# Optimization experiments

Hardware: AMD Instinct MI355X
Metric: run time of the kernel (lower is better)

The kernel has to match this reference:

```python
import jax, jax.numpy as jnp
from jax import lax
import numpy as np

B, IMG, PS = 64, 384, 16
DM, DS, DI = 96, 16, 96
DT_RANK = 6
NREP = 4
NCLS = 5
HP = IMG // PS            # 24 patches per side
N = HP * HP               # 576 tokens


def _ln(x, g, b):
    m = x.mean(-1, keepdims=True)
    v = ((x - m) ** 2).mean(-1, keepdims=True)
    return (x - m) * lax.rsqrt(v + 1e-5) * g + b


def setup_inputs() -> dict:
    key = jax.random.key(0)
    ks = jax.random.split(key, 16)
    nrm = lambda k, s: jax.random.normal(k, s, jnp.float32) * 0.02
    return {
        "x": jax.random.uniform(ks[0], (B, 3, IMG, IMG), jnp.float32),
        "W_pe": nrm(ks[1], (DM, 3, PS, PS)), "b_pe": jnp.zeros((DM,), jnp.float32),
        "W_vis": nrm(ks[2], (DM, 1)), "b_vis": jnp.zeros((1,), jnp.float32),
        "dn_g": jnp.ones((DM,), jnp.float32), "dn_b": jnp.zeros((DM,), jnp.float32),
        "W_gate": nrm(ks[3], (DM, DM)), "b_gate": jnp.zeros((DM,), jnp.float32),
        "ln_g": jnp.ones((DM,), jnp.float32), "ln_b": jnp.zeros((DM,), jnp.float32),
        "W_in": nrm(ks[4], (DM, 2 * DI)),
        "conv_w": nrm(ks[5], (DI, 1, 3)),
        "W_xproj": nrm(ks[6], (DI, DT_RANK + 2 * DS)),
        "W_dt": nrm(ks[7], (DT_RANK, DI)), "b_dt": jnp.full((DI,), -2.0, jnp.float32),
        "A_log": jnp.log(jnp.tile(jnp.arange(1, DS + 1, dtype=jnp.float32), (DI, 1))),
        "D": jnp.ones((DI,), jnp.float32),
        "W_out": nrm(ks[8], (DI, DM)),
        "hd_dw": nrm(ks[9], (DM, 1, 3, 3)),
        "bn_g": jnp.ones((DM,), jnp.float32), "bn_b": jnp.zeros((DM,), jnp.float32),
        "bn_m": jnp.zeros((DM,), jnp.float32), "bn_v": jnp.ones((DM,), jnp.float32),
        "W_heat": nrm(ks[10], (NCLS, DM)), "b_heat": jnp.full((NCLS,), -2.19, jnp.float32),
        "W_off": nrm(ks[11], (2, DM)), "b_off": jnp.zeros((2,), jnp.float32),
        "W_size": nrm(ks[12], (2, DM)), "b_size": jnp.zeros((2,), jnp.float32),
    }


def _forward(x, W_pe, b_pe, W_vis, b_vis, dn_g, dn_b, W_gate, b_gate,
             ln_g, ln_b, W_in, conv_w, W_xproj, W_dt, b_dt, A_log, D, W_out,
             hd_dw, bn_g, bn_b, bn_m, bn_v, W_heat, b_heat, W_off, b_off, W_size, b_size):
    # --- retinex preprocessing (single-scale, log domain) ---
    kblur = jnp.ones((3, 1, 5, 5), jnp.float32) / 25.0
    L = lax.conv_general_dilated(x, kblur, (1, 1), 'SAME',
                                 feature_group_count=3,
                                 dimension_numbers=('NCHW', 'OIHW', 'NCHW'))
    x = jnp.log1p(jnp.clip(x, 0.0)) - jnp.log1p(jnp.clip(L, 0.0))
    # --- patch embedding: strided conv -> tokens (B,N,DM) ---
    t = lax.conv_general_dilated(x, W_pe, (PS, PS), 'VALID',
                                 dimension_numbers=('NCHW', 'OIHW', 'NCHW'))
    t = t + b_pe[None, :, None, None]
    tokens = t.reshape(B, DM, N).transpose(0, 2, 1)
    # --- visibility estimator: per-token gate (B,N,1) ---
    vis = jax.nn.sigmoid(tokens @ W_vis + b_vis)
    # --- dual norm: LN + sigmoid gate ---
    tokens = _ln(tokens, dn_g, dn_b)
    norm_gate = jax.nn.sigmoid(tokens @ W_gate + b_gate)  # (B,N,DM)
    # --- weight-shared NC-SSM blocks ---
    A = -jnp.exp(A_log)  # (DI,DS)
    for _ in range(NREP):
        resid = tokens
        h = _ln(tokens, ln_g, ln_b)
        xz = h @ W_in                      # (B,N,2*DI)
        xin, z = xz[..., :DI], xz[..., DI:]
        # causal depthwise conv1d over sequence, kernel 3
        xc = xin.transpose(0, 2, 1)        # (B,DI,N)
        xc = lax.conv_general_dilated(xc, conv_w, (1,), [(2, 0)],
                                      feature_group_count=DI,
                                      dimension_numbers=('NCH', 'OIH', 'NCH'))
        xs = jax.nn.silu(xc.transpose(0, 2, 1))  # (B,N,DI)
        # selective-scan parameters
        proj = xs @ W_xproj                # (B,N,DT_RANK+2*DS)
        dt_raw = proj[..., :DT_RANK]
        Bc = proj[..., DT_RANK:DT_RANK + DS]
        Cc = proj[..., DT_RANK + DS:]
        dt = jax.nn.softplus(dt_raw @ W_dt + b_dt)  # (B,N,DI)
        # time-major scan
        def step(hst, inp):
            dt_t, B_t, C_t, x_t = inp      # (B,DI),(B,DS),(B,DS),(B,DI)
            dA = jnp.exp(dt_t[:, :, None] * A)                 # (B,DI,DS)
            hst = dA * hst + (dt_t * x_t)[:, :, None] * B_t[:, None, :]
            y = jnp.einsum('bds,bs->bd', hst, C_t)
            return hst, y
        h0 = jnp.zeros((B, DI, DS), jnp.float32)
        _, ys = lax.scan(step, h0, (dt.transpose(1, 0, 2), Bc.transpose(1, 0, 2),
                                    Cc.transpose(1, 0, 2), xs.transpose(1, 0, 2)))
        y = ys.transpose(1, 0, 2) + D * xs           # (B,N,DI)
        y = y * jax.nn.silu(z) * vis                  # gated by z and visibility
        tokens = resid + (y @ W_out) * norm_gate
    # --- CenterNet-style head ---
    f = tokens.transpose(0, 2, 1).reshape(B, DM, HP, HP)
    g = lax.conv_general_dilated(f, hd_dw, (1, 1), 'SAME',
                                 feature_group_count=DM,
                                 dimension_numbers=('NCHW', 'OIHW', 'NCHW'))
    g = (g - bn_m[None, :, None, None]) * lax.rsqrt(bn_v + 1e-5)[None, :, None, None]
    g = jax.nn.silu(g * bn_g[None, :, None, None] + bn_b[None, :, None, None])
    heat = jnp.einsum('bchw,oc->bohw', g, W_heat) + b_heat[None, :, None, None]
    off = jnp.einsum('bchw,oc->bohw', f, W_off) + b_off[None, :, None, None]
    size = jnp.einsum('bchw,oc->bohw', f, W_size) + b_size[None, :, None, None]
    return heat, off, size


def reference(x, W_pe, b_pe, W_vis, b_vis, dn_g, dn_b, W_gate, b_gate,
              ln_g, ln_b, W_in, conv_w, W_xproj, W_dt, b_dt, A_log, D, W_out,
              hd_dw, bn_g, bn_b, bn_m, bn_v, W_heat, b_heat, W_off, b_off, W_size, b_size):
    return _forward(x, W_pe, b_pe, W_vis, b_vis, dn_g, dn_b, W_gate, b_gate,
                    ln_g, ln_b, W_in, conv_w, W_xproj, W_dt, b_dt, A_log, D, W_out,
                    hd_dw, bn_g, bn_b, bn_m, bn_v, W_heat, b_heat, W_off, b_off,
                    W_size, b_size)
```

## Files before the change

### kernel.cpp

```cpp
#include <hip/hip_runtime.h>

#define DEVINL __device__ __forceinline__

typedef __attribute__((ext_vector_type(8))) short bf8v;
typedef __attribute__((ext_vector_type(4))) float f4v;

DEVINL float b2f(unsigned short u){ union{unsigned int i; float f;} x; x.i = ((unsigned int)u)<<16; return x.f; }
DEVINL unsigned short f2b(float f){ union{float f; unsigned int i;} x; x.f = f; unsigned int r = x.i + 0x7FFFu + ((x.i>>16)&1u); return (unsigned short)(r>>16); }
DEVINL float sigf(float v){ return 1.f/(1.f + __expf(-v)); }
DEVINL void unpack8(const uint4 u, float* d){
  d[0]=b2f((unsigned short)(u.x)); d[1]=b2f((unsigned short)(u.x>>16));
  d[2]=b2f((unsigned short)(u.y)); d[3]=b2f((unsigned short)(u.y>>16));
  d[4]=b2f((unsigned short)(u.z)); d[5]=b2f((unsigned short)(u.z>>16));
  d[6]=b2f((unsigned short)(u.w)); d[7]=b2f((unsigned short)(u.w>>16));
}
DEVINL uint4 pack8(const float* s){
  uint4 u;
  u.x = (unsigned int)f2b(s[0]) | ((unsigned int)f2b(s[1])<<16);
  u.y = (unsigned int)f2b(s[2]) | ((unsigned int)f2b(s[3])<<16);
  u.z = (unsigned int)f2b(s[4]) | ((unsigned int)f2b(s[5])<<16);
  u.w = (unsigned int)f2b(s[6]) | ((unsigned int)f2b(s[7])<<16);
  return u;
}
union FragU { uint4 u; bf8v v; };


#define WS_XLOG   ((size_t)0)
#define WS_TOKRAW ((size_t)56623104)
#define WS_VIS    ((size_t)70778880)
#define WS_WGT    ((size_t)70926336)
#define WS_WIT    ((size_t)70944768)
#define WS_WXT    ((size_t)70981632)
#define WS_WOT    ((size_t)71006208)
#define WS_AMAT   ((size_t)71024640)
#define WS_WPE    ((size_t)71030784)
#define WS_CW     ((size_t)71178240)
#define WS_TOK    ((size_t)0)
#define WS_GATE   ((size_t)14155776)
#define WS_XSB    ((size_t)21233664)
#define WS_Y2     ((size_t)28311552)
#define WS_XIN    ((size_t)35389440)
#define WS_ZSV    ((size_t)42467328)
#define WS_DT     ((size_t)49545216)
#define WS_BC     ((size_t)56623104)

#define PREP_STRIDE (128*256)
__global__ __launch_bounds__(256) void k_prep(
    const float* __restrict__ Wgate, const float* __restrict__ Win,
    const float* __restrict__ Wxproj, const float* __restrict__ Wdt,
    const float* __restrict__ Wout, const float* __restrict__ Alog,
    const float* __restrict__ Wpe, const float* __restrict__ convw,
    unsigned short* __restrict__ WgT, unsigned short* __restrict__ WiT,
    unsigned short* __restrict__ WxT, unsigned short* __restrict__ WoT,
    float* __restrict__ Amat, unsigned short* __restrict__ WpeB,
    float* __restrict__ cwsplit)
{
  int gtid = blockIdx.x*256 + threadIdx.x;
  for (int i = gtid; i < 9216; i += PREP_STRIDE){
    int n = i/96, k = i - n*96;
    WgT[n*96+k] = f2b(Wgate[k*96+n]);
    WoT[n*96+k] = f2b(Wout[k*96+n]);
  }
  for (int i = gtid; i < 18432; i += PREP_STRIDE){
    int n = i/96, k = i - n*96;
    WiT[n*96+k] = f2b(Win[k*192+n]);
  }
  for (int i = gtid; i < 12288; i += PREP_STRIDE){
    int n = i/96, k = i - n*96;
    if (n < 96){
      float s = 0.f;
      for (int r = 0; r < 6; ++r) s += Wxproj[k*38+r] * Wdt[r*96+n];
      WxT[n*96+k] = f2b(s);
    } else {
      WxT[n*96+k] = f2b(Wxproj[k*38 + 6 + (n-96)]);
    }
  }
  for (int i = gtid; i < 1536; i += PREP_STRIDE) Amat[i] = -__expf(Alog[i]);
  for (int i = gtid; i < 73728; i += PREP_STRIDE) WpeB[i] = f2b(Wpe[i]);
  for (int i = gtid; i < 96; i += PREP_STRIDE){
    cwsplit[i]       = convw[i*3+0];
    cwsplit[96+i]    = convw[i*3+1];
    cwsplit[192+i]   = convw[i*3+2];
  }
}

__global__ __launch_bounds__(256) void k_blur(const float* __restrict__ x,
                                              unsigned short* __restrict__ xlog)
{
  __shared__ float xt[12*384];
  int bid = blockIdx.x;
  int tile = bid % 48; int bc = bid / 48; int c = bc % 3; int b = bc / 3;
  const float* xin = x + (size_t)(b*3 + c) * 147456;
  unsigned short* xout = xlog + (size_t)(b*3 + c) * 147456;
  int y0 = tile * 8;
  int tid = threadIdx.x;

  #pragma unroll
  for (int k = 0; k < 5; ++k){
    int idx = tid + k*256;
    if (idx < 1152){
      int r = idx / 96; int c4 = idx - r*96;
      int gy = y0 - 2 + r;
      float4 v = make_float4(0.f,0.f,0.f,0.f);
      if (gy >= 0 && gy < 384) v = *(const float4*)(xin + gy*384 + c4*4);
      *(float4*)(xt + r*384 + c4*4) = v;
    }
  }
  __syncthreads();

  #pragma unroll
  for (int k = 0; k < 2; ++k){
    int slot = tid + k*256;
    int r = slot >> 6; int c8 = slot & 63;
    bool act = (c8 < 48);
    float vs[8];
    if (act){
      const float* base = xt + r*384 + c8*8;
      float4 a0 = *(const float4*)(base);
      float4 a1 = *(const float4*)(base + 4);
      vs[0]=a0.x; vs[1]=a0.y; vs[2]=a0.z; vs[3]=a0.w;
      vs[4]=a1.x; vs[5]=a1.y; vs[6]=a1.z; vs[7]=a1.w;
      #pragma unroll
      for (int i = 1; i < 5; ++i){
        float4 p = *(const float4*)(base + i*384);
        float4 q = *(const float4*)(base + i*384 + 4);
        vs[0]+=p.x; vs[1]+=p.y; vs[2]+=p.z; vs[3]+=p.w;
        vs[4]+=q.x; vs[5]+=q.y; vs[6]+=q.z; vs[7]+=q.w;
      }
    } else {
      #pragma unroll
      for (int j = 0; j < 8; ++j) vs[j] = 0.f;
    }
    float l2 = __shfl_up(vs[6], 1);
    float l1 = __shfl_up(vs[7], 1);
    float r1 = __shfl_down(vs[0], 1);
    float r2 = __shfl_down(vs[1], 1);
    if (c8 == 0){ l2 = 0.f; l1 = 0.f; }
    if (c8 == 47){ r1 = 0.f; r2 = 0.f; }
    if (act){
      float e[12];
      e[0]=l2; e[1]=l1;
      #pragma unroll
      for (int j = 0; j < 8; ++j) e[2+j] = vs[j];
      e[10]=r1; e[11]=r2;
      const float* xraw = xt + (r+2)*384 + c8*8;
      float xv[8];
      *(float4*)(xv)   = *(const float4*)(xraw);
      *(float4*)(xv+4) = *(const float4*)(xraw + 4);
      float res[8];
      #pragma unroll
      for (int j = 0; j < 8; ++j){
        float s = ((e[j]+e[j+1]) + (e[j+2]+e[j+3])) + e[j+4];
        float L = fmaxf(s * 0.04f, 0.f);
        float xc = fmaxf(xv[j], 0.f);
        res[j] = __logf(1.f + xc) - __logf(1.f + L);
      }
      *(uint4*)(xout + (y0+r)*384 + c8*8) = pack8(res);
    }
  }
}

__global__ __launch_bounds__(256) void k_patch(const unsigned short* __restrict__ xlog,
    const unsigned short* __restrict__ WpeB, const float* __restrict__ bpe,
    float* __restrict__ tokraw)
{
  int wid = threadIdx.x >> 6, lane = threadIdx.x & 63;
  int gid = blockIdx.x*4 + wid;
  int tile = gid >> 1, half = gid & 1;
  int m0 = tile*16;
  int nf0 = half*3;
  int l15 = lane & 15, q = lane >> 4;
  int ma0 = m0 + l15;
  int b0 = ma0/576; int r0 = ma0 - b0*576; int hp0 = r0/24; int wp0 = r0 - hp0*24;
  size_t base0 = (size_t)b0*442368 + (size_t)hp0*6144 + (size_t)wp0*16;
  f4v acc[3];
  #pragma unroll
  for (int j=0;j<3;++j)
    #pragma unroll
    for (int r=0;r<4;++r) acc[j][r] = 0.f;
  for (int ks = 0; ks < 24; ++ks){
    int k0 = ks*32 + q*8;
    int c  = k0 >> 8;
    int ph = (k0 >> 4) & 15;
    int pw = k0 & 15;
    size_t off = (size_t)c*147456 + (size_t)ph*384 + pw;
    bf8v a0 = *(const bf8v*)(xlog + base0 + off);
    #pragma unroll
    for (int nf = 0; nf < 3; ++nf){
      bf8v bb = *(const bf8v*)(WpeB + (size_t)((nf0+nf)*16 + l15)*768 + k0);
      acc[nf] = __builtin_amdgcn_mfma_f32_16x16x32_bf16(a0, bb, acc[nf], 0, 0, 0);
    }
  }
  #pragma unroll
  for (int nf=0; nf<3; ++nf)
    #pragma unroll
    for (int r=0; r<4; ++r){
      int m = m0 + q*4 + r;
      int n = (nf0+nf)*16 + l15;
      tokraw[(size_t)m*96 + n] = acc[nf][r] + bpe[n];
    }
}

__global__ __launch_bounds__(256) void k_lngate(const float* __restrict__ in,
    const float* __restrict__ g, const float* __restrict__ bta,
    const float* __restrict__ Wvis, const float* __restrict__ bvis,
    const unsigned short* __restrict__ BT, const float* __restrict__ bg,
    float* __restrict__ tokout, unsigned short* __restrict__ gate,
    float* __restrict__ vis)
{
  int wid = threadIdx.x >> 6, lane = threadIdx.x & 63;
  int gid = blockIdx.x*4 + wid;
  int tile = gid >> 1, half = gid & 1;
  int m0 = tile*16;
  int nf0 = half*3;
  int l15 = lane & 15, q = lane >> 4;
  int ma0 = m0 + l15;
  float a0v[24];
  float s0=0.f, w0=0.f, vd=0.f;
  #pragma unroll
  for (int ks = 0; ks < 3; ++ks){
    int k0 = ks*32 + q*8;
    #pragma unroll
    for (int h = 0; h < 2; ++h){
      float4 va = *(const float4*)(in + (size_t)ma0*96 + k0 + h*4);
      float4 wv = *(const float4*)(Wvis + k0 + h*4);
      int o = ks*8 + h*4;
      a0v[o+0]=va.x; a0v[o+1]=va.y; a0v[o+2]=va.z; a0v[o+3]=va.w;
      s0 += (va.x+va.y)+(va.z+va.w);
      w0 += (va.x*va.x+va.y*va.y)+(va.z*va.z+va.w*va.w);
      vd += (va.x*wv.x+va.y*wv.y)+(va.z*wv.z+va.w*wv.w);
    }
  }
  s0 += __shfl_xor(s0, 16); s0 += __shfl_xor(s0, 32);
  w0 += __shfl_xor(w0, 16); w0 += __shfl_xor(w0, 32);
  vd += __shfl_xor(vd, 16); vd += __shfl_xor(vd, 32);
  float mu0 = s0*(1.f/96.f);
  float rs0 = rsqrtf(fmaxf(w0*(1.f/96.f)-mu0*mu0, 0.f) + 1e-5f);
  if (half == 0 && q == 0) vis[ma0] = sigf(vd + bvis[0]);

  bf8v fa0[3];
  #pragma unroll
  for (int ks = 0; ks < 3; ++ks){
    int k0 = ks*32 + q*8;
    float gv[8], bv[8];
    *(float4*)(gv)   = *(const float4*)(g + k0);
    *(float4*)(gv+4) = *(const float4*)(g + k0 + 4);
    *(float4*)(bv)   = *(const float4*)(bta + k0);
    *(float4*)(bv+4) = *(const float4*)(bta + k0 + 4);
    float v0[8];
    #pragma unroll
    for (int j = 0; j < 8; ++j){
      v0[j] = (a0v[ks*8+j]-mu0)*rs0*gv[j] + bv[j];
    }
    if (half == 0){
      *(float4*)(tokout + (size_t)ma0*96 + k0)     = make_float4(v0[0],v0[1],v0[2],v0[3]);
      *(float4*)(tokout + (size_t)ma0*96 + k0 + 4) = make_float4(v0[4],v0[5],v0[6],v0[7]);
    }
    FragU U0; U0.u = pack8(v0);
    fa0[ks] = U0.v;
  }

  f4v acc[3];
  #pragma unroll
  for (int j=0;j<3;++j)
    #pragma unroll
    for (int r=0;r<4;++r) acc[j][r] = 0.f;
  const bf8v* bp = (const bf8v*)(BT) + (size_t)l15*12 + q;
  #pragma unroll
  for (int ks = 0; ks < 3; ++ks){
    #pragma unroll
    for (int nf = 0; nf < 3; ++nf){
      bf8v bb = bp[(nf0+nf)*192 + ks*4];
      acc[nf] = __builtin_amdgcn_mfma_f32_16x16x32_bf16(fa0[ks], bb, acc[nf], 0, 0, 0);
    }
  }
  #pragma unroll
  for (int nf=0; nf<3; ++nf)
    #pragma unroll
    for (int r=0; r<4; ++r){
      int m = m0 + q*4 + r;
      int n = (nf0+nf)*16 + l15;
      gate[(size_t)m*96 + n] = f2b(sigf(acc[nf][r] + bg[n]));
    }
}

template<int NF, class Epi>
__global__ __launch_bounds__(256) void tokgemm96(const unsigned short* __restrict__ A,
    const unsigned short* __restrict__ BT, Epi epi)
{
  constexpr int NF2 = NF/2;
  int wid = threadIdx.x >> 6, lane = threadIdx.x & 63;
  int gid = blockIdx.x*4 + wid;
  int tile = gid >> 1, half = gid & 1;
  int m0 = tile*16;
  int nf0 = half*NF2;
  int l15 = lane & 15, q = lane >> 4;
  f4v acc[NF2];
  #pragma unroll
  for (int j=0;j<NF2;++j)
    #pragma unroll
    for (int r=0;r<4;++r) acc[j][r] = 0.f;
  const bf8v* a0p = (const bf8v*)(A) + (size_t)(m0 + l15)*12 + q;
  const bf8v* bp  = (const bf8v*)(BT) + (size_t)l15*12 + q;
  #pragma unroll
  for (int ks = 0; ks < 3; ++ks){
    bf8v a0 = a0p[ks*4];
    #pragma unroll
    for (int nf = 0; nf < NF2; ++nf){
      bf8v bb = bp[(nf0+nf)*192 + ks*4];
      acc[nf] = __builtin_amdgcn_mfma_f32_16x16x32_bf16(a0, bb, acc[nf], 0, 0, 0);
    }
  }
  #pragma unroll
  for (int nf=0; nf<NF2; ++nf)
    #pragma unroll
    for (int r=0; r<4; ++r)
      epi(m0 + q*4 + r, (nf0+nf)*16 + l15, acc[nf][r]);
}

struct WoutEpi {
  const unsigned short* gate; float* tokens;
  __device__ void operator()(int m, int n, float v) const {
    size_t i = (size_t)m*96 + n;
    tokens[i] = tokens[i] + v * b2f(gate[i]);
  }
};

__global__ __launch_bounds__(256) void k_lnwin(const float* __restrict__ tokp,
    const float* __restrict__ lng, const float* __restrict__ lnb,
    const unsigned short* __restrict__ BT, const float* __restrict__ vis,
    unsigned short* __restrict__ xin, unsigned short* __restrict__ zsv)
{
  int wid = threadIdx.x >> 6, lane = threadIdx.x & 63;
  int gid = blockIdx.x*4 + wid;
  int tile = gid >> 1, half = gid & 1;
  int m0 = tile*16;
  int nf0 = half*6;
  int l15 = lane & 15, q = lane >> 4;
  int ma0 = m0 + l15;
  float a0v[24];
  float s0=0.f, w0=0.f;
  #pragma unroll
  for (int ks = 0; ks < 3; ++ks){
    int k0 = ks*32 + q*8;
    #pragma unroll
    for (int h = 0; h < 2; ++h){
      float4 va = *(const float4*)(tokp + (size_t)ma0*96 + k0 + h*4);
      int o = ks*8 + h*4;
      a0v[o+0]=va.x; a0v[o+1]=va.y; a0v[o+2]=va.z; a0v[o+3]=va.w;
      s0 += (va.x+va.y)+(va.z+va.w);
      w0 += (va.x*va.x+va.y*va.y)+(va.z*va.z+va.w*va.w);
    }
  }
  s0 += __shfl_xor(s0, 16); s0 += __shfl_xor(s0, 32);
  w0 += __shfl_xor(w0, 16); w0 += __shfl_xor(w0, 32);
  float mu0 = s0*(1.f/96.f);
  float rs0 = rsqrtf(fmaxf(w0*(1.f/96.f)-mu0*mu0, 0.f) + 1e-5f);

  bf8v fa0[3];
  #pragma unroll
  for (int ks = 0; ks < 3; ++ks){
    int k0 = ks*32 + q*8;
    float gv[8], bv[8];
    *(float4*)(gv)   = *(const float4*)(lng + k0);
    *(float4*)(gv+4) = *(const float4*)(lng + k0 + 4);
    *(float4*)(bv)   = *(const float4*)(lnb + k0);
    *(float4*)(bv+4) = *(const float4*)(lnb + k0 + 4);
    float v0[8];
    #pragma unroll
    for (int j = 0; j < 8; ++j){
      v0[j] = (a0v[ks*8+j]-mu0)*rs0*gv[j] + bv[j];
    }
    FragU U0; U0.u = pack8(v0);
    fa0[ks] = U0.v;
  }

  f4v acc[6];
  #pragma unroll
  for (int j=0;j<6;++j)
    #pragma unroll
    for (int r=0;r<4;++r) acc[j][r] = 0.f;
  const bf8v* bp = (const bf8v*)(BT) + (size_t)l15*12 + q;
  #pragma unroll
  for (int ks = 0; ks < 3; ++ks){
    #pragma unroll
    for (int nf = 0; nf < 6; ++nf){
      bf8v bb = bp[(nf0+nf)*192 + ks*4];
      acc[nf] = __builtin_amdgcn_mfma_f32_16x16x32_bf16(fa0[ks], bb, acc[nf], 0, 0, 0);
    }
  }
  if (half == 0){
    #pragma unroll
    for (int nf=0; nf<6; ++nf)
      #pragma unroll
      for (int r=0; r<4; ++r){
        int m = m0 + q*4 + r;
        int n = nf*16 + l15;
        xin[(size_t)m*96 + n] = f2b(acc[nf][r]);
      }
  } else {
    #pragma unroll
    for (int nf=0; nf<6; ++nf)
      #pragma unroll
      for (int r=0; r<4; ++r){
        int m = m0 + q*4 + r;
        int n = (6+nf)*16 + l15;
        float v = acc[nf][r];
        float s = v * sigf(v);
        zsv[(size_t)m*96 + (n-96)] = f2b(s * vis[m]);
      }
  }
}

__global__ __launch_bounds__(256) void k_convxp(const unsigned short* __restrict__ xinb,
    const float* __restrict__ cwsplit, const unsigned short* __restrict__ BT,
    const float* __restrict__ bdt, unsigned short* __restrict__ xsb,
    unsigned short* __restrict__ dt, unsigned short* __restrict__ bc)
{
  int wid = threadIdx.x >> 6, lane = threadIdx.x & 63;
  int gid = blockIdx.x*4 + wid;
  int tile = gid >> 1, half = gid & 1;
  int m0 = tile*16;
  int nf0 = half*4;
  int l15 = lane & 15, q = lane >> 4;
  int ma0 = m0 + l15;
  int t0 = ma0 % 576;
  const float* cw0 = cwsplit;
  const float* cw1 = cwsplit + 96;
  const float* cw2 = cwsplit + 192;

  bf8v fa0[3];
  uint4 z4 = make_uint4(0,0,0,0);
  #pragma unroll
  for (int ks = 0; ks < 3; ++ks){
    int k0 = ks*32 + q*8;
    const unsigned short* r0p = xinb + (size_t)ma0*96 + k0;
    uint4 c0u  = *(const uint4*)(r0p);
    uint4 p10u = (t0 >= 1) ? *(const uint4*)(r0p - 96)  : z4;
    uint4 p20u = (t0 >= 2) ? *(const uint4*)(r0p - 192) : z4;
    float fc0[8], fp10[8], fp20[8];
    unpack8(c0u, fc0); unpack8(p10u, fp10); unpack8(p20u, fp20);
    float w0v[8], w1v[8], w2v[8];
    *(float4*)(w0v)   = *(const float4*)(cw0 + k0);
    *(float4*)(w0v+4) = *(const float4*)(cw0 + k0 + 4);
    *(float4*)(w1v)   = *(const float4*)(cw1 + k0);
    *(float4*)(w1v+4) = *(const float4*)(cw1 + k0 + 4);
    *(float4*)(w2v)   = *(const float4*)(cw2 + k0);
    *(float4*)(w2v+4) = *(const float4*)(cw2 + k0 + 4);
    float xs0[8];
    #pragma unroll
    for (int j = 0; j < 8; ++j){
      float v0 = w2v[j]*fc0[j] + w1v[j]*fp10[j] + w0v[j]*fp20[j];
      xs0[j] = v0 * sigf(v0);
    }
    FragU U0; U0.u = pack8(xs0);
    fa0[ks] = U0.v;
    if (half == 0) *(uint4*)(xsb + (size_t)ma0*96 + k0) = U0.u;
  }

  f4v acc[4];
  #pragma unroll
  for (int j=0;j<4;++j)
    #pragma unroll
    for (int r=0;r<4;++r) acc[j][r] = 0.f;
  const bf8v* bp = (const bf8v*)(BT) + (size_t)l15*12 + q;
  #pragma unroll
  for (int ks = 0; ks < 3; ++ks){
    #pragma unroll
    for (int nf = 0; nf < 4; ++nf){
      bf8v bb = bp[(nf0+nf)*192 + ks*4];
      acc[nf] = __builtin_amdgcn_mfma_f32_16x16x32_bf16(fa0[ks], bb, acc[nf], 0, 0, 0);
    }
  }
  #pragma unroll
  for (int nf=0; nf<4; ++nf)
    #pragma unroll
    for (int r=0; r<4; ++r){
      int m = m0 + q*4 + r;
      int n = (nf0+nf)*16 + l15;
      float v = acc[nf][r];
      if (n < 96){
        float xx = v + bdt[n];
        float sp = (xx > 20.f) ? xx : __logf(1.f + __expf(xx));
        dt[(size_t)m*96 + n] = f2b(sp);
      } else {
        bc[(size_t)m*32 + (n-96)] = f2b(v);
      }
    }
}

__global__ __launch_bounds__(512) void k_scan(const unsigned short* __restrict__ dt,
    const unsigned short* __restrict__ xsb, const unsigned short* __restrict__ bc,
    const unsigned short* __restrict__ zsv, const float* __restrict__ Amat,
// ... 143 lines not shown
  int b = blockIdx.x / 24; int h = blockIdx.x - b*24;
  for (int i = threadIdx.x; i < 3*2304; i += 256){
    int rr = i / 2304; int j = i - rr*2304;
    int hh = h + rr - 1;
    float v = 0.f;
    if (hh >= 0 && hh < 24) v = tokens[((size_t)b*576 + hh*24)*96 + j];
    ft[rr*2304 + j] = v;
  }
  __syncthreads();
  for (int i = threadIdx.x; i < 2304; i += 256){
    int w = i / 96; int cc = i - w*96;
    float g = 0.f;
    #pragma unroll
    for (int dh = 0; dh < 3; ++dh){
      #pragma unroll
      for (int dw = 0; dw < 3; ++dw){
        int ww = w + dw - 1;
        if (ww >= 0 && ww < 24) g += ft[dh*2304 + ww*96 + cc] * hdw[cc*9 + dh*3 + dw];
      }
    }
    float gn = (g - bnm[cc]) * rsqrtf(bnv[cc] + 1e-5f);
    float a = gn * bng[cc] + bnb[cc];
    act[i] = a * sigf(a);
  }
  __syncthreads();
  int tid = threadIdx.x;
  if (tid < 120){
    int o = tid / 24; int w = tid - o*24;
    float s = 0.f;
    for (int cc = 0; cc < 96; ++cc) s += act[w*96 + cc] * Wheat[o*96 + cc];
    s += bheat[o];
    out[(size_t)b*2880 + o*576 + h*24 + w] = s;
  } else if (tid >= 128 && tid < 224){
    int idx = tid - 128; int o2 = idx / 24; int w = idx - o2*24;
    const float* W = (o2 < 2) ? Woff : Wsize;
    int o = o2 & 1;
    float s = 0.f;
    for (int cc = 0; cc < 96; ++cc) s += ft[2304 + w*96 + cc] * W[o*96 + cc];
    s += ((o2 < 2) ? boff : bsize)[o];
    size_t baseo = (o2 < 2) ? (size_t)184320 : (size_t)258048;
    out[baseo + (size_t)b*1152 + o*576 + h*24 + w] = s;
  }
}

extern "C" void kernel_launch(void* const* d_in, const int* in_sizes, int n_in,
                              void* d_out, int out_size, void* d_ws, size_t ws_size,
                              hipStream_t stream)
{
  (void)in_sizes; (void)n_in; (void)out_size; (void)ws_size;
  const float* x      = (const float*)d_in[0];
  const float* Wpe    = (const float*)d_in[1];
  const float* bpe    = (const float*)d_in[2];
  const float* Wvis   = (const float*)d_in[3];
  const float* bvis   = (const float*)d_in[4];
  const float* dng    = (const float*)d_in[5];
  const float* dnb    = (const float*)d_in[6];
  const float* Wgate  = (const float*)d_in[7];
  const float* bgate  = (const float*)d_in[8];
  const float* lng    = (const float*)d_in[9];
  const float* lnb    = (const float*)d_in[10];
  const float* Win    = (const float*)d_in[11];
  const float* convw  = (const float*)d_in[12];
  const float* Wxproj = (const float*)d_in[13];
  const float* Wdt    = (const float*)d_in[14];
  const float* bdt    = (const float*)d_in[15];
  const float* Alog   = (const float*)d_in[16];
  const float* Dw     = (const float*)d_in[17];
  const float* Wout   = (const float*)d_in[18];
  const float* hddw   = (const float*)d_in[19];
  const float* bng    = (const float*)d_in[20];
  const float* bnb    = (const float*)d_in[21];
  const float* bnm    = (const float*)d_in[22];
  const float* bnv    = (const float*)d_in[23];
  const float* Wheat  = (const float*)d_in[24];
  const float* bheat  = (const float*)d_in[25];
  const float* Woff   = (const float*)d_in[26];
  const float* boff   = (const float*)d_in[27];
  const float* Wsize  = (const float*)d_in[28];
  const float* bsize  = (const float*)d_in[29];
  float* out = (float*)d_out;

  char* ws = (char*)d_ws;
  unsigned short* xlog  = (unsigned short*)(ws + WS_XLOG);
  float*          tokraw= (float*)(ws + WS_TOKRAW);
  float*          vis   = (float*)(ws + WS_VIS);
  unsigned short* WgT   = (unsigned short*)(ws + WS_WGT);
  unsigned short* WiT   = (unsigned short*)(ws + WS_WIT);
  unsigned short* WxT   = (unsigned short*)(ws + WS_WXT);
  unsigned short* WoT   = (unsigned short*)(ws + WS_WOT);
  float*          Amat  = (float*)(ws + WS_AMAT);
  unsigned short* WpeB  = (unsigned short*)(ws + WS_WPE);
  float*          cwsp  = (float*)(ws + WS_CW);
  float*          tok   = (float*)(ws + WS_TOK);
  unsigned short* gate  = (unsigned short*)(ws + WS_GATE);
  unsigned short* xsb   = (unsigned short*)(ws + WS_XSB);
  unsigned short* y2    = (unsigned short*)(ws + WS_Y2);
  unsigned short* xinb  = (unsigned short*)(ws + WS_XIN);
  unsigned short* zsvb  = (unsigned short*)(ws + WS_ZSV);
  unsigned short* dtb   = (unsigned short*)(ws + WS_DT);
  unsigned short* bcb   = (unsigned short*)(ws + WS_BC);

  k_prep<<<128, 256, 0, stream>>>(Wgate, Win, Wxproj, Wdt, Wout, Alog, Wpe, convw,
                                  WgT, WiT, WxT, WoT, Amat, WpeB, cwsp);
  k_blur<<<9216, 256, 0, stream>>>(x, xlog);
  k_patch<<<1152, 256, 0, stream>>>(xlog, WpeB, bpe, tokraw);
  k_lngate<<<1152, 256, 0, stream>>>(tokraw, dng, dnb, Wvis, bvis, WgT, bgate,
                                     tok, gate, vis);

  for (int rep = 0; rep < 4; ++rep){
    k_lnwin<<<1152, 256, 0, stream>>>(tok, lng, lnb, WiT, vis, xinb, zsvb);
    k_convxp<<<1152, 256, 0, stream>>>(xinb, cwsp, WxT, bdt, xsb, dtb, bcb);
    k_scan<<<384, 512, 0, stream>>>(dtb, xsb, bcb, zsvb, Amat, Dw, y2);
    tokgemm96<6, WoutEpi><<<1152, 256, 0, stream>>>(y2, WoT, WoutEpi{gate, tok});
  }

  k_head<<<1536, 256, 0, stream>>>(tok, hddw, bng, bnb, bnm, bnv,
                                   Wheat, bheat, Woff, boff, Wsize, bsize, out);
}
```

Baseline: 699.5 us.

## Fuse patch-embed with LayerNorm, and Wout residual with next LN+in-proj

Several kernel boundaries are merged. The patch-embed GEMM now computes all 96 output columns per wave so it can apply the first LayerNorm and the vis projection in registers, writing tok directly. The gate GEMM is fused with the first LN+W_in pass. Each Wout residual update now also runs the next repetition's LayerNorm and in-projection from LDS, which removes a kernel launch and a full re-read of tok per repetition. The blur stages the input tile as bf16 in LDS with a separate horizontal pass, trading input precision for less LDS, and the workspace layout is reshuffled.

```diff
diff --git a/kernel.cpp b/kernel.cpp
--- a/kernel.cpp
+++ b/kernel.cpp
@@ -26,7 +26,7 @@
 
 
 #define WS_XLOG   ((size_t)0)
-#define WS_TOKRAW ((size_t)56623104)
+#define WS_TOK    ((size_t)56623104)
 #define WS_VIS    ((size_t)70778880)
 #define WS_WGT    ((size_t)70926336)
 #define WS_WIT    ((size_t)70944768)
@@ -35,14 +35,13 @@
 #define WS_AMAT   ((size_t)71024640)
 #define WS_WPE    ((size_t)71030784)
 #define WS_CW     ((size_t)71178240)
-#define WS_TOK    ((size_t)0)
+#define WS_BC     ((size_t)0)
 #define WS_GATE   ((size_t)14155776)
 #define WS_XSB    ((size_t)21233664)
 #define WS_Y2     ((size_t)28311552)
 #define WS_XIN    ((size_t)35389440)
 #define WS_ZSV    ((size_t)42467328)
 #define WS_DT     ((size_t)49545216)
-#define WS_BC     ((size_t)56623104)
 
 #define PREP_STRIDE (128*256)
 __global__ __launch_bounds__(256) void k_prep(
@@ -87,7 +86,8 @@
 __global__ __launch_bounds__(256) void k_blur(const float* __restrict__ x,
                                               unsigned short* __restrict__ xlog)
 {
-  __shared__ float xt[12*384];
+  __shared__ unsigned short xt[12*384];
+  __shared__ float vt[8*392];
   int bid = blockIdx.x;
   int tile = bid % 48; int bc = bid / 48; int c = bc % 3; int b = bc / 3;
   const float* xin = x + (size_t)(b*3 + c) * 147456;
@@ -103,79 +103,78 @@
       int gy = y0 - 2 + r;
       float4 v = make_float4(0.f,0.f,0.f,0.f);
       if (gy >= 0 && gy < 384) v = *(const float4*)(xin + gy*384 + c4*4);
-      *(float4*)(xt + r*384 + c4*4) = v;
-    }
+      ushort4 o; o.x=f2b(v.x); o.y=f2b(v.y); o.z=f2b(v.z); o.w=f2b(v.w);
+      *(ushort4*)(xt + r*384 + c4*4) = o;
+    }
+  }
+  if (tid < 64){
+    int r = tid >> 3; int j = tid & 7;
+    vt[r*392 + ((j < 4) ? j : (384 + j))] = 0.f;
   }
   __syncthreads();
 
   #pragma unroll
   for (int k = 0; k < 2; ++k){
-    int slot = tid + k*256;
-    int r = slot >> 6; int c8 = slot & 63;
-    bool act = (c8 < 48);
-    float vs[8];
-    if (act){
-      const float* base = xt + r*384 + c8*8;
-      float4 a0 = *(const float4*)(base);
-      float4 a1 = *(const float4*)(base + 4);
-      vs[0]=a0.x; vs[1]=a0.y; vs[2]=a0.z; vs[3]=a0.w;
-      vs[4]=a1.x; vs[5]=a1.y; vs[6]=a1.z; vs[7]=a1.w;
+    int unit = tid + k*256;
+    if (unit < 384){
+      int r = unit / 48; int c8 = unit - r*48;
+      const unsigned short* base = xt + r*384 + c8*8;
+      float acc[8]; float t[8];
+      uint4 u0 = *(const uint4*)(base);
+      unpack8(u0, acc);
       #pragma unroll
       for (int i = 1; i < 5; ++i){
-        float4 p = *(const float4*)(base + i*384);
-        float4 q = *(const float4*)(base + i*384 + 4);
-        vs[0]+=p.x; vs[1]+=p.y; vs[2]+=p.z; vs[3]+=p.w;
-        vs[4]+=q.x; vs[5]+=q.y; vs[6]+=q.z; vs[7]+=q.w;
-      }
-    } else {
-      #pragma unroll
-      for (int j = 0; j < 8; ++j) vs[j] = 0.f;
-    }
-    float l2 = __shfl_up(vs[6], 1);
-    float l1 = __shfl_up(vs[7], 1);
-    float r1 = __shfl_down(vs[0], 1);
-    float r2 = __shfl_down(vs[1], 1);
-    if (c8 == 0){ l2 = 0.f; l1 = 0.f; }
-    if (c8 == 47){ r1 = 0.f; r2 = 0.f; }
-    if (act){
-      float e[12];
-      e[0]=l2; e[1]=l1;
-      #pragma unroll
-      for (int j = 0; j < 8; ++j) e[2+j] = vs[j];
-      e[10]=r1; e[11]=r2;
-      const float* xraw = xt + (r+2)*384 + c8*8;
-      float xv[8];
-      *(float4*)(xv)   = *(const float4*)(xraw);
-      *(float4*)(xv+4) = *(const float4*)(xraw + 4);
-      float res[8];
-      #pragma unroll
-      for (int j = 0; j < 8; ++j){
-        float s = ((e[j]+e[j+1]) + (e[j+2]+e[j+3])) + e[j+4];
-        float L = fmaxf(s * 0.04f, 0.f);
-        float xc = fmaxf(xv[j], 0.f);
-        res[j] = __logf(1.f + xc) - __logf(1.f + L);
-      }
-      *(uint4*)(xout + (y0+r)*384 + c8*8) = pack8(res);
-    }
-  }
-}
-
-__global__ __launch_bounds__(256) void k_patch(const unsigned short* __restrict__ xlog,
-    const unsigned short* __restrict__ WpeB, const float* __restrict__ bpe,
-    float* __restrict__ tokraw)
+        uint4 u = *(const uint4*)(base + i*384);
+        unpack8(u, t);
+        #pragma unroll
+        for (int j = 0; j < 8; ++j) acc[j] += t[j];
+      }
+      float* vrow = vt + r*392 + 4 + c8*8;
+      *(float4*)(vrow)   = make_float4(acc[0],acc[1],acc[2],acc[3]);
+      *(float4*)(vrow+4) = make_float4(acc[4],acc[5],acc[6],acc[7]);
+    }
+  }
+  __syncthreads();
+
+  #pragma unroll
+  for (int k = 0; k < 3; ++k){
+    int unit = tid + k*256;
+    int r = unit / 96; int c4 = unit - r*96;
+    int base = r*392 + 4 + c4*4;
+    float f[12];
+    *(float4*)(f)   = *(const float4*)(vt + base - 4);
+    *(float4*)(f+4) = *(const float4*)(vt + base);
+    *(float4*)(f+8) = *(const float4*)(vt + base + 4);
+    ushort4 xr = *(const ushort4*)(xt + (r+2)*384 + c4*4);
+    const unsigned short* xrp = &xr.x;
+    ushort4 o;
+    unsigned short* op = &o.x;
+    #pragma unroll
+    for (int j = 0; j < 4; ++j){
+      float s = f[2+j] + f[3+j] + f[4+j] + f[5+j] + f[6+j];
+      float L = fmaxf(s * 0.04f, 0.f);
+      float xv = fmaxf(b2f(xrp[j]), 0.f);
+      op[j] = f2b(__logf(1.f + xv) - __logf(1.f + L));
+    }
+    *(ushort4*)(xout + (y0+r)*384 + c4*4) = o;
+  }
+}
+
+__global__ __launch_bounds__(256) void k_patchln(
+    const unsigned short* __restrict__ xlog, const unsigned short* __restrict__ WpeB,
+    const float* __restrict__ bpe, const float* __restrict__ dng,
+    const float* __restrict__ dnb, const float* __restrict__ Wvis,
+    const float* __restrict__ bvis, float* __restrict__ tok, float* __restrict__ vis)
 {
   int wid = threadIdx.x >> 6, lane = threadIdx.x & 63;
-  int gid = blockIdx.x*4 + wid;
-  int tile = gid >> 1, half = gid & 1;
-  int m0 = tile*16;
-  int nf0 = half*3;
+  int m0 = (blockIdx.x*4 + wid)*16;
   int l15 = lane & 15, q = lane >> 4;
   int ma0 = m0 + l15;
   int b0 = ma0/576; int r0 = ma0 - b0*576; int hp0 = r0/24; int wp0 = r0 - hp0*24;
   size_t base0 = (size_t)b0*442368 + (size_t)hp0*6144 + (size_t)wp0*16;
-  f4v acc[3];
-  #pragma unroll
-  for (int j=0;j<3;++j)
+  f4v acc[6];
+  #pragma unroll
+  for (int j=0;j<6;++j)
     #pragma unroll
     for (int r=0;r<4;++r) acc[j][r] = 0.f;
   for (int ks = 0; ks < 24; ++ks){
@@ -186,178 +185,93 @@
     size_t off = (size_t)c*147456 + (size_t)ph*384 + pw;
     bf8v a0 = *(const bf8v*)(xlog + base0 + off);
     #pragma unroll
-    for (int nf = 0; nf < 3; ++nf){
-      bf8v bb = *(const bf8v*)(WpeB + (size_t)((nf0+nf)*16 + l15)*768 + k0);
+    for (int nf = 0; nf < 6; ++nf){
+      bf8v bb = *(const bf8v*)(WpeB + (size_t)(nf*16 + l15)*768 + k0);
       acc[nf] = __builtin_amdgcn_mfma_f32_16x16x32_bf16(a0, bb, acc[nf], 0, 0, 0);
     }
   }
-  #pragma unroll
-  for (int nf=0; nf<3; ++nf)
-    #pragma unroll
-    for (int r=0; r<4; ++r){
-      int m = m0 + q*4 + r;
-      int n = (nf0+nf)*16 + l15;
-      tokraw[(size_t)m*96 + n] = acc[nf][r] + bpe[n];
-    }
-}
-
-__global__ __launch_bounds__(256) void k_lngate(const float* __restrict__ in,
-    const float* __restrict__ g, const float* __restrict__ bta,
-    const float* __restrict__ Wvis, const float* __restrict__ bvis,
-    const unsigned short* __restrict__ BT, const float* __restrict__ bg,
-    float* __restrict__ tokout, unsigned short* __restrict__ gate,
-    float* __restrict__ vis)
+  float v[6][4];
+  float s[4], w[4], vd[4];
+  #pragma unroll
+  for (int r=0;r<4;++r){ s[r]=0.f; w[r]=0.f; vd[r]=0.f; }
+  #pragma unroll
+  for (int nf=0; nf<6; ++nf){
+    int n = nf*16 + l15;
+    float bp = bpe[n];
+    float wv = Wvis[n];
+    #pragma unroll
+    for (int r=0;r<4;++r){
+      float t = acc[nf][r] + bp;
+      v[nf][r] = t;
+      s[r] += t; w[r] += t*t; vd[r] += t*wv;
+    }
+  }
+  #pragma unroll
+  for (int off=1; off<16; off<<=1){
+    #pragma unroll
+    for (int r=0;r<4;++r){
+      s[r]  += __shfl_xor(s[r],  off);
+      w[r]  += __shfl_xor(w[r],  off);
+      vd[r] += __shfl_xor(vd[r], off);
+    }
+  }
+  float mu[4], rs[4];
+  #pragma unroll
+  for (int r=0;r<4;++r){
+    mu[r] = s[r]*(1.f/96.f);
+    rs[r] = rsqrtf(fmaxf(w[r]*(1.f/96.f)-mu[r]*mu[r], 0.f) + 1e-5f);
+  }
+  if (l15 == 0){
+    #pragma unroll
+    for (int r=0;r<4;++r) vis[m0 + q*4 + r] = sigf(vd[r] + bvis[0]);
+  }
+  #pragma unroll
+  for (int nf=0; nf<6; ++nf){
+    int n = nf*16 + l15;
+    float g = dng[n], bb = dnb[n];
+    #pragma unroll
+    for (int r=0;r<4;++r)
+      tok[(size_t)(m0 + q*4 + r)*96 + n] = (v[nf][r]-mu[r])*rs[r]*g + bb;
+  }
+}
+
+__global__ __launch_bounds__(256) void k_lnfull(const float* __restrict__ tokp,
+    const unsigned short* __restrict__ WgT, const float* __restrict__ bg,
+    const float* __restrict__ lng, const float* __restrict__ lnb,
+    const unsigned short* __restrict__ WiT, const float* __restrict__ vis,
+    unsigned short* __restrict__ gate, unsigned short* __restrict__ xin,
+    unsigned short* __restrict__ zsv)
 {
   int wid = threadIdx.x >> 6, lane = threadIdx.x & 63;
   int gid = blockIdx.x*4 + wid;
   int tile = gid >> 1, half = gid & 1;
   int m0 = tile*16;
-  int nf0 = half*3;
   int l15 = lane & 15, q = lane >> 4;
   int ma0 = m0 + l15;
   float a0v[24];
-  float s0=0.f, w0=0.f, vd=0.f;
+  float s1=0.f, w1=0.f;
+  bf8v fa[3];
   #pragma unroll
   for (int ks = 0; ks < 3; ++ks){
     int k0 = ks*32 + q*8;
-    #pragma unroll
-    for (int h = 0; h < 2; ++h){
-      float4 va = *(const float4*)(in + (size_t)ma0*96 + k0 + h*4);
-      float4 wv = *(const float4*)(Wvis + k0 + h*4);
-      int o = ks*8 + h*4;
-      a0v[o+0]=va.x; a0v[o+1]=va.y; a0v[o+2]=va.z; a0v[o+3]=va.w;
-      s0 += (va.x+va.y)+(va.z+va.w);
-      w0 += (va.x*va.x+va.y*va.y)+(va.z*va.z+va.w*va.w);
-      vd += (va.x*wv.x+va.y*wv.y)+(va.z*wv.z+va.w*wv.w);
-    }
-  }
-  s0 += __shfl_xor(s0, 16); s0 += __shfl_xor(s0, 32);
-  w0 += __shfl_xor(w0, 16); w0 += __shfl_xor(w0, 32);
-  vd += __shfl_xor(vd, 16); vd += __shfl_xor(vd, 32);
-  float mu0 = s0*(1.f/96.f);
-  float rs0 = rsqrtf(fmaxf(w0*(1.f/96.f)-mu0*mu0, 0.f) + 1e-5f);
-  if (half == 0 && q == 0) vis[ma0] = sigf(vd + bvis[0]);
-
-  bf8v fa0[3];
-  #pragma unroll
-  for (int ks = 0; ks < 3; ++ks){
-    int k0 = ks*32 + q*8;
-    float gv[8], bv[8];
-    *(float4*)(gv)   = *(const float4*)(g + k0);
-    *(float4*)(gv+4) = *(const float4*)(g + k0 + 4);
-    *(float4*)(bv)   = *(const float4*)(bta + k0);
-    *(float4*)(bv+4) = *(const float4*)(bta + k0 + 4);
     float v0[8];
-    #pragma unroll
-    for (int j = 0; j < 8; ++j){
-      v0[j] = (a0v[ks*8+j]-mu0)*rs0*gv[j] + bv[j];
-    }
-    if (half == 0){
-      *(float4*)(tokout + (size_t)ma0*96 + k0)     = make_float4(v0[0],v0[1],v0[2],v0[3]);
-      *(float4*)(tokout + (size_t)ma0*96 + k0 + 4) = make_float4(v0[4],v0[5],v0[6],v0[7]);
-    }
-    FragU U0; U0.u = pack8(v0);
-    fa0[ks] = U0.v;
-  }
-
-  f4v acc[3];
-  #pragma unroll
-  for (int j=0;j<3;++j)
-    #pragma unroll
-    for (int r=0;r<4;++r) acc[j][r] = 0.f;
-  const bf8v* bp = (const bf8v*)(BT) + (size_t)l15*12 + q;
-  #pragma unroll
-  for (int ks = 0; ks < 3; ++ks){
-    #pragma unroll
-    for (int nf = 0; nf < 3; ++nf){
-      bf8v bb = bp[(nf0+nf)*192 + ks*4];
-      acc[nf] = __builtin_amdgcn_mfma_f32_16x16x32_bf16(fa0[ks], bb, acc[nf], 0, 0, 0);
-    }
-  }
-  #pragma unroll
-  for (int nf=0; nf<3; ++nf)
-    #pragma unroll
-    for (int r=0; r<4; ++r){
-      int m = m0 + q*4 + r;
-      int n = (nf0+nf)*16 + l15;
-      gate[(size_t)m*96 + n] = f2b(sigf(acc[nf][r] + bg[n]));
-    }
-}
-
-template<int NF, class Epi>
-__global__ __launch_bounds__(256) void tokgemm96(const unsigned short* __restrict__ A,
-    const unsigned short* __restrict__ BT, Epi epi)
-{
-  constexpr int NF2 = NF/2;
-  int wid = threadIdx.x >> 6, lane = threadIdx.x & 63;
-  int gid = blockIdx.x*4 + wid;
-  int tile = gid >> 1, half = gid & 1;
-  int m0 = tile*16;
-  int nf0 = half*NF2;
-  int l15 = lane & 15, q = lane >> 4;
-  f4v acc[NF2];
-  #pragma unroll
-  for (int j=0;j<NF2;++j)
-    #pragma unroll
-    for (int r=0;r<4;++r) acc[j][r] = 0.f;
-  const bf8v* a0p = (const bf8v*)(A) + (size_t)(m0 + l15)*12 + q;
-  const bf8v* bp  = (const bf8v*)(BT) + (size_t)l15*12 + q;
-  #pragma unroll
-  for (int ks = 0; ks < 3; ++ks){
-    bf8v a0 = a0p[ks*4];
-    #pragma unroll
-    for (int nf = 0; nf < NF2; ++nf){
-      bf8v bb = bp[(nf0+nf)*192 + ks*4];
-      acc[nf] = __builtin_amdgcn_mfma_f32_16x16x32_bf16(a0, bb, acc[nf], 0, 0, 0);
-    }
-  }
-  #pragma unroll
-  for (int nf=0; nf<NF2; ++nf)
-    #pragma unroll
-    for (int r=0; r<4; ++r)
-      epi(m0 + q*4 + r, (nf0+nf)*16 + l15, acc[nf][r]);
-}
-
-struct WoutEpi {
-  const unsigned short* gate; float* tokens;
-  __device__ void operator()(int m, int n, float v) const {
-    size_t i = (size_t)m*96 + n;
-    tokens[i] = tokens[i] + v * b2f(gate[i]);
-  }
-};
-
-__global__ __launch_bounds__(256) void k_lnwin(const float* __restrict__ tokp,
-    const float* __restrict__ lng, const float* __restrict__ lnb,
-    const unsigned short* __restrict__ BT, const float* __restrict__ vis,
-    unsigned short* __restrict__ xin, unsigned short* __restrict__ zsv)
-{
-  int wid = threadIdx.x >> 6, lane = threadIdx.x & 63;
-  int gid = blockIdx.x*4 + wid;
-  int tile = gid >> 1, half = gid & 1;
-  int m0 = tile*16;
-  int nf0 = half*6;
-  int l15 = lane & 15, q = lane >> 4;
-  int ma0 = m0 + l15;
-  float a0v[24];
-  float s0=0.f, w0=0.f;
-  #pragma unroll
-  for (int ks = 0; ks < 3; ++ks){
-    int k0 = ks*32 + q*8;
     #pragma unroll
     for (int h = 0; h < 2; ++h){
       float4 va = *(const float4*)(tokp + (size_t)ma0*96 + k0 + h*4);
       int o = ks*8 + h*4;
       a0v[o+0]=va.x; a0v[o+1]=va.y; a0v[o+2]=va.z; a0v[o+3]=va.w;
-      s0 += (va.x+va.y)+(va.z+va.w);
-      w0 += (va.x*va.x+va.y*va.y)+(va.z*va.z+va.w*va.w);
-    }
-  }
-  s0 += __shfl_xor(s0, 16); s0 += __shfl_xor(s0, 32);
-  w0 += __shfl_xor(w0, 16); w0 += __shfl_xor(w0, 32);
-  float mu0 = s0*(1.f/96.f);
-  float rs0 = rsqrtf(fmaxf(w0*(1.f/96.f)-mu0*mu0, 0.f) + 1e-5f);
-
-  bf8v fa0[3];
+      v0[h*4+0]=va.x; v0[h*4+1]=va.y; v0[h*4+2]=va.z; v0[h*4+3]=va.w;
+      s1 += (va.x+va.y)+(va.z+va.w);
+      w1 += (va.x*va.x+va.y*va.y)+(va.z*va.z+va.w*va.w);
+    }
+    FragU U0; U0.u = pack8(v0);
+    fa[ks] = U0.v;
+  }
+  s1 += __shfl_xor(s1, 16); s1 += __shfl_xor(s1, 32);
+  w1 += __shfl_xor(w1, 16); w1 += __shfl_xor(w1, 32);
+  float mu1 = s1*(1.f/96.f);
+  float rs1 = rsqrtf(fmaxf(w1*(1.f/96.f)-mu1*mu1, 0.f) + 1e-5f);
+  bf8v fb[3];
   #pragma unroll
   for (int ks = 0; ks < 3; ++ks){
     int k0 = ks*32 + q*8;
@@ -368,47 +282,190 @@
     *(float4*)(bv+4) = *(const float4*)(lnb + k0 + 4);
     float v0[8];
     #pragma unroll
-    for (int j = 0; j < 8; ++j){
-      v0[j] = (a0v[ks*8+j]-mu0)*rs0*gv[j] + bv[j];
-    }
+    for (int j = 0; j < 8; ++j)
+      v0[j] = (a0v[ks*8+j]-mu1)*rs1*gv[j] + bv[j];
     FragU U0; U0.u = pack8(v0);
-    fa0[ks] = U0.v;
-  }
-
-  f4v acc[6];
-  #pragma unroll
-  for (int j=0;j<6;++j)
-    #pragma unroll
-    for (int r=0;r<4;++r) acc[j][r] = 0.f;
-  const bf8v* bp = (const bf8v*)(BT) + (size_t)l15*12 + q;
-  #pragma unroll
-  for (int ks = 0; ks < 3; ++ks){
-    #pragma unroll
-    for (int nf = 0; nf < 6; ++nf){
-      bf8v bb = bp[(nf0+nf)*192 + ks*4];
-      acc[nf] = __builtin_amdgcn_mfma_f32_16x16x32_bf16(fa0[ks], bb, acc[nf], 0, 0, 0);
-    }
-  }
-  if (half == 0){
-    #pragma unroll
-    for (int nf=0; nf<6; ++nf)
+    fb[ks] = U0.v;
+  }
+
+  {
+    f4v ag[3];
+    #pragma unroll
+    for (int j=0;j<3;++j)
+      #pragma unroll
+      for (int r=0;r<4;++r) ag[j][r] = 0.f;
+    const bf8v* bpg = (const bf8v*)(WgT) + (size_t)l15*12 + q;
+    #pragma unroll
+    for (int ks = 0; ks < 3; ++ks)
+      #pragma unroll
+      for (int nf = 0; nf < 3; ++nf){
+        bf8v bb = bpg[(half*3+nf)*192 + ks*4];
+        ag[nf] = __builtin_amdgcn_mfma_f32_16x16x32_bf16(fa[ks], bb, ag[nf], 0, 0, 0);
+      }
+    #pragma unroll
+    for (int nf=0; nf<3; ++nf)
       #pragma unroll
       for (int r=0; r<4; ++r){
         int m = m0 + q*4 + r;
-        int n = nf*16 + l15;
-        xin[(size_t)m*96 + n] = f2b(acc[nf][r]);
-      }
-  } else {
-    #pragma unroll
-    for (int nf=0; nf<6; ++nf)
-      #pragma unroll
-      for (int r=0; r<4; ++r){
-        int m = m0 + q*4 + r;
-        int n = (6+nf)*16 + l15;
-        float v = acc[nf][r];
-        float s = v * sigf(v);
-        zsv[(size_t)m*96 + (n-96)] = f2b(s * vis[m]);
-      }
+        int n = (half*3+nf)*16 + l15;
+        gate[(size_t)m*96 + n] = f2b(sigf(ag[nf][r] + bg[n]));
+      }
+  }
+
+  {
+    f4v aw[6];
+    #pragma unroll
+    for (int j=0;j<6;++j)
+      #pragma unroll
+      for (int r=0;r<4;++r) aw[j][r] = 0.f;
+    const bf8v* bpw = (const bf8v*)(WiT) + (size_t)l15*12 + q;
+    #pragma unroll
+    for (int ks = 0; ks < 3; ++ks)
+      #pragma unroll
+      for (int nf = 0; nf < 6; ++nf){
+        bf8v bb = bpw[(half*6+nf)*192 + ks*4];
+        aw[nf] = __builtin_amdgcn_mfma_f32_16x16x32_bf16(fb[ks], bb, aw[nf], 0, 0, 0);
+      }
+    if (half == 0){
+      #pragma unroll
+      for (int nf=0; nf<6; ++nf)
+        #pragma unroll
+        for (int r=0; r<4; ++r){
+          int m = m0 + q*4 + r;
+          int n = nf*16 + l15;
+          xin[(size_t)m*96 + n] = f2b(aw[nf][r]);
+        }
+    } else {
+      #pragma unroll
+      for (int nf=0; nf<6; ++nf)
+        #pragma unroll
+        for (int r=0; r<4; ++r){
+          int m = m0 + q*4 + r;
+          int n = nf*16 + l15;
+          float v = aw[nf][r];
+          float sgl = v * sigf(v);
+          zsv[(size_t)m*96 + n] = f2b(sgl * vis[m]);
+        }
+    }
+  }
+}
+
+template<bool DOLN>
+__global__ __launch_bounds__(256) void k_woutln(
+    const unsigned short* __restrict__ y2, const unsigned short* __restrict__ WoT,
+    const unsigned short* __restrict__ gate,
+    const float* __restrict__ lng, const float* __restrict__ lnb,
+    const unsigned short* __restrict__ WiT, const float* __restrict__ vis,
+    float* __restrict__ tok, unsigned short* __restrict__ xin,
+    unsigned short* __restrict__ zsv)
+{
+  __shared__ float Sl[2][16][100];
+  int wid = threadIdx.x >> 6, lane = threadIdx.x & 63;
+  int gid = blockIdx.x*4 + wid;
+  int tile = gid >> 1, half = gid & 1;
+  int tl = wid >> 1;
+  int m0 = tile*16;
+  int l15 = lane & 15, q = lane >> 4;
+
+  f4v acc[3];
+  #pragma unroll
+  for (int j=0;j<3;++j)
+    #pragma unroll
+    for (int r=0;r<4;++r) acc[j][r] = 0.f;
+  const bf8v* a0p = (const bf8v*)(y2) + (size_t)(m0 + l15)*12 + q;
+  const bf8v* bp  = (const bf8v*)(WoT) + (size_t)l15*12 + q;
+  #pragma unroll
+  for (int ks = 0; ks < 3; ++ks){
+    bf8v a0 = a0p[ks*4];
+    #pragma unroll
+    for (int nf = 0; nf < 3; ++nf){
+      bf8v bb = bp[(half*3+nf)*192 + ks*4];
+      acc[nf] = __builtin_amdgcn_mfma_f32_16x16x32_bf16(a0, bb, acc[nf], 0, 0, 0);
+    }
+  }
+  #pragma unroll
+  for (int nf=0; nf<3; ++nf)
+    #pragma unroll
+    for (int r=0; r<4; ++r){
+      int m = m0 + q*4 + r;
+      int n = (half*3+nf)*16 + l15;
+      size_t i = (size_t)m*96 + n;
+      float tn = tok[i] + acc[nf][r] * b2f(gate[i]);
+      tok[i] = tn;
+      if constexpr (DOLN) Sl[tl][q*4+r][n] = tn;
+    }
+
+  if constexpr (DOLN){
+    __syncthreads();
+    int ma0 = m0 + l15;
+    float a0v[24];
+    float s0=0.f, w0=0.f;
+    #pragma unroll
+    for (int ks = 0; ks < 3; ++ks){
+      int k0 = ks*32 + q*8;
+      #pragma unroll
+      for (int h = 0; h < 2; ++h){
+        float4 va = *(const float4*)(&Sl[tl][l15][k0 + h*4]);
+        int o = ks*8 + h*4;
+        a0v[o+0]=va.x; a0v[o+1]=va.y; a0v[o+2]=va.z; a0v[o+3]=va.w;
+        s0 += (va.x+va.y)+(va.z+va.w);
+        w0 += (va.x*va.x+va.y*va.y)+(va.z*va.z+va.w*va.w);
+      }
+    }
+    s0 += __shfl_xor(s0, 16); s0 += __shfl_xor(s0, 32);
+    w0 += __shfl_xor(w0, 16); w0 += __shfl_xor(w0, 32);
+    float mu0 = s0*(1.f/96.f);
+    float rs0 = rsqrtf(fmaxf(w0*(1.f/96.f)-mu0*mu0, 0.f) + 1e-5f);
+    bf8v fb[3];
+    #pragma unroll
+    for (int ks = 0; ks < 3; ++ks){
+      int k0 = ks*32 + q*8;
+      float gv[8], bv[8];
+      *(float4*)(gv)   = *(const float4*)(lng + k0);
+      *(float4*)(gv+4) = *(const float4*)(lng + k0 + 4);
+      *(float4*)(bv)   = *(const float4*)(lnb + k0);
+      *(float4*)(bv+4) = *(const float4*)(lnb + k0 + 4);
+      float v0[8];
+      #pragma unroll
+      for (int j = 0; j < 8; ++j)
+        v0[j] = (a0v[ks*8+j]-mu0)*rs0*gv[j] + bv[j];
+      FragU U0; U0.u = pack8(v0);
+      fb[ks] = U0.v;
+    }
+    f4v aw[6];
+    #pragma unroll
+    for (int j=0;j<6;++j)
+      #pragma unroll
+      for (int r=0;r<4;++r) aw[j][r] = 0.f;
+    const bf8v* bpw = (const bf8v*)(WiT) + (size_t)l15*12 + q;
+    #pragma unroll
+    for (int ks = 0; ks < 3; ++ks)
+      #pragma unroll
+      for (int nf = 0; nf < 6; ++nf){
+        bf8v bb = bpw[(half*6+nf)*192 + ks*4];
+        aw[nf] = __builtin_amdgcn_mfma_f32_16x16x32_bf16(fb[ks], bb, aw[nf], 0, 0, 0);
+      }
+    if (half == 0){
+      #pragma unroll
+      for (int nf=0; nf<6; ++nf)
+        #pragma unroll
+        for (int r=0; r<4; ++r){
+          int m = m0 + q*4 + r;
+          int n = nf*16 + l15;
+          xin[(size_t)m*96 + n] = f2b(aw[nf][r]);
+        }
+    } else {
+      #pragma unroll
+      for (int nf=0; nf<6; ++nf)
+        #pragma unroll
+        for (int r=0; r<4; ++r){
+          int m = m0 + q*4 + r;
+          int n = nf*16 + l15;
+          float v = aw[nf][r];
+          float sgl = v * sigf(v);
+          zsv[(size_t)m*96 + n] = f2b(sgl * vis[m]);
+        }
+    }
   }
 }
 
@@ -718,7 +775,7 @@
 
   char* ws = (char*)d_ws;
   unsigned short* xlog  = (unsigned short*)(ws + WS_XLOG);
-  float*          tokraw= (float*)(ws + WS_TOKRAW);
+  float*          tok   = (float*)(ws + WS_TOK);
   float*          vis   = (float*)(ws + WS_VIS);
   unsigned short* WgT   = (unsigned short*)(ws + WS_WGT);
   unsigned short* WiT   = (unsigned short*)(ws + WS_WIT);
@@ -727,27 +784,30 @@
   float*          Amat  = (float*)(ws + WS_AMAT);
   unsigned short* WpeB  = (unsigned short*)(ws + WS_WPE);
   float*          cwsp  = (float*)(ws + WS_CW);
-  float*          tok   = (float*)(ws + WS_TOK);
+  unsigned short* bcb   = (unsigned short*)(ws + WS_BC);
   unsigned short* gate  = (unsigned short*)(ws + WS_GATE);
   unsigned short* xsb   = (unsigned short*)(ws + WS_XSB);
   unsigned short* y2    = (unsigned short*)(ws + WS_Y2);
   unsigned short* xinb  = (unsigned short*)(ws + WS_XIN);
   unsigned short* zsvb  = (unsigned short*)(ws + WS_ZSV);
   unsigned short* dtb   = (unsigned short*)(ws + WS_DT);
-  unsigned short* bcb   = (unsigned short*)(ws + WS_BC);
 
   k_prep<<<128, 256, 0, stream>>>(Wgate, Win, Wxproj, Wdt, Wout, Alog, Wpe, convw,
                                   WgT, WiT, WxT, WoT, Amat, WpeB, cwsp);
   k_blur<<<9216, 256, 0, stream>>>(x, xlog);
-  k_patch<<<1152, 256, 0, stream>>>(xlog, WpeB, bpe, tokraw);
-  k_lngate<<<1152, 256, 0, stream>>>(tokraw, dng, dnb, Wvis, bvis, WgT, bgate,
-                                     tok, gate, vis);
+  k_patchln<<<576, 256, 0, stream>>>(xlog, WpeB, bpe, dng, dnb, Wvis, bvis, tok, vis);
+  k_lnfull<<<1152, 256, 0, stream>>>(tok, WgT, bgate, lng, lnb, WiT, vis,
+                                     gate, xinb, zsvb);
 
   for (int rep = 0; rep < 4; ++rep){
-    k_lnwin<<<1152, 256, 0, stream>>>(tok, lng, lnb, WiT, vis, xinb, zsvb);
     k_convxp<<<1152, 256, 0, stream>>>(xinb, cwsp, WxT, bdt, xsb, dtb, bcb);
     k_scan<<<384, 512, 0, stream>>>(dtb, xsb, bcb, zsvb, Amat, Dw, y2);
-    tokgemm96<6, WoutEpi><<<1152, 256, 0, stream>>>(y2, WoT, WoutEpi{gate, tok});
+    if (rep < 3)
+      k_woutln<true><<<1152, 256, 0, stream>>>(y2, WoT, gate, lng, lnb, WiT, vis,
+                                               tok, xinb, zsvb);
+    else
+      k_woutln<false><<<1152, 256, 0, stream>>>(y2, WoT, gate, lng, lnb, WiT, vis,
+                                                tok, xinb, zsvb);
   }
 
   k_head<<<1536, 256, 0, stream>>>(tok, hddw, bng, bnb, bnm, bnv,
```

After: 671.7 us. -4.0%, faster.
